# Kernel tuning notes

Measured on AMD Instinct MI355X. Metric: run time of the kernel, lower is better.

Reference implementation:

```python
import jax, jax.numpy as jnp
import numpy as np

B, C, H, W = 128, 256, 32, 32
TD, NHEADS, PH, PW = 192, 4, 4, 4
FF = 384
MAXG = 8
TABLE = (2 * MAXG - 1) ** 2  # 225


def setup_inputs() -> dict:
    key = jax.random.key(0)
    ks = jax.random.split(key, 10)
    rn = lambda k, shape, s=0.02: jax.random.normal(k, shape, jnp.float32) * s
    return {
        "x": jax.random.normal(ks[0], (B, C, H, W), jnp.float32),
        "conv1_w": rn(ks[1], (TD, C)),          # 1x1 conv, no bias
        "conv2_w": rn(ks[2], (C, TD)),          # 1x1 conv, no bias
        "qkv_w": rn(ks[3], (TD, 3 * TD)), "qkv_b": jnp.zeros((3 * TD,), jnp.float32),
        "proj_w": rn(ks[4], (TD, TD)), "proj_b": jnp.zeros((TD,), jnp.float32),
        "ffn_w1": rn(ks[5], (TD, FF)), "ffn_b1": jnp.zeros((FF,), jnp.float32),
        "ffn_w2": rn(ks[6], (FF, TD)), "ffn_b2": jnp.zeros((TD,), jnp.float32),
        "ln1_g": jnp.ones((TD,), jnp.float32), "ln1_b": jnp.zeros((TD,), jnp.float32),
        "ln2_g": jnp.ones((TD,), jnp.float32), "ln2_b": jnp.zeros((TD,), jnp.float32),
        "alpha": rn(ks[7], (1,), 0.1),
        "rpb_table": rn(ks[8], (TABLE, NHEADS)),
    }


def _ln(x, g, b, eps=1e-5):
    m = x.mean(-1, keepdims=True)
    v = ((x - m) ** 2).mean(-1, keepdims=True)
    return (x - m) * jax.lax.rsqrt(v + eps) * g + b


def _rpb_index(Nh, Nw, maxg):
    # static (trace-time) relative position index over the patch grid
    ch, cw = np.meshgrid(np.arange(Nh), np.arange(Nw), indexing="ij")
    coords = np.stack([ch.ravel(), cw.ravel()])                 # (2, N)
    rel = coords[:, :, None] - coords[:, None, :]               # (2, N, N)
    idx = (rel[0] + maxg - 1) * (2 * maxg - 1) + (rel[1] + maxg - 1)
    return jnp.asarray(idx.reshape(-1), jnp.int32)              # (N*N,)


def reference(x, conv1_w, conv2_w, qkv_w, qkv_b, proj_w, proj_b,
              ffn_w1, ffn_b1, ffn_w2, ffn_b2,
              ln1_g, ln1_b, ln2_g, ln2_b, alpha, rpb_table):
    Nh, Nw = H // PH, W // PW
    Np = Nh * Nw
    hd = TD // NHEADS
    scale = 1.0 / np.sqrt(hd).astype(np.float32)

    # local 1x1 conv
    xl = jnp.einsum("bchw,tc->bthw", x, conv1_w)                # (B, TD, H, W)
    # patchify + mean-pool -> one token per patch
    xp = xl.reshape(B, TD, Nh, PH, Nw, PW).transpose(0, 2, 4, 3, 5, 1)
    xp = xp.reshape(B, Np, PH * PW, TD)
    tokens = xp.mean(axis=2)                                    # (B, Np, TD)

    # attention with gathered relative position bias
    t = _ln(tokens, ln1_g, ln1_b)
    qkv = (t @ qkv_w + qkv_b).reshape(B, Np, 3, NHEADS, hd)
    q, k, v = qkv[:, :, 0], qkv[:, :, 1], qkv[:, :, 2]          # (B, Np, H, hd)
    attn = jnp.einsum("bnhd,bmhd->bhnm", q, k) * scale
    bias = rpb_table[_rpb_index(Nh, Nw, MAXG)]                  # (Np*Np, heads)
    bias = bias.reshape(Np, Np, NHEADS).transpose(2, 0, 1)      # (heads, Np, Np)
    attn = jax.nn.softmax(attn + bias[None], axis=-1)
    o = jnp.einsum("bhnm,bmhd->bnhd", attn, v).reshape(B, Np, TD)
    o = o @ proj_w + proj_b

    out = tokens + alpha * o                                    # scaled residual
    h2 = _ln(out, ln2_g, ln2_b)
    out = out + (jax.nn.gelu(h2 @ ffn_w1 + ffn_b1, approximate=False) @ ffn_w2 + ffn_b2)

    # unpatchify: broadcast each token back over its ph*pw pixels
    ot = jnp.broadcast_to(out[:, :, None, :], (B, Np, PH * PW, TD))
    ot = ot.reshape(B, Nh, Nw, PH, PW, TD).transpose(0, 5, 1, 3, 2, 4)
    ot = ot.reshape(B, TD, H, W)
    return x + jnp.einsum("bthw,ct->bchw", ot, conv2_w)
```

## Files before the change

### kernel.cpp

```cpp
#include <hip/hip_runtime.h>
#include <hip/hip_bf16.h>

#define Bsz 128
#define Cch 256
#define Him 32
#define Wim 32
#define TD 192
#define NH 4
#define HD 48
#define FF 384
#define NP 64

typedef float f32x4 __attribute__((ext_vector_type(4)));
typedef __bf16 bf16x8 __attribute__((ext_vector_type(8)));
typedef unsigned int u32;

#define MFMA(a, b, c) __builtin_amdgcn_mfma_f32_16x16x32_bf16(a, b, c, 0, 0, 0)
#define LD8(p) (*reinterpret_cast<const bf16x8*>(p))
#define VM0 asm volatile("s_waitcnt vmcnt(0)" ::: "memory")
#define VM2 asm volatile("s_waitcnt vmcnt(2)" ::: "memory")
#define VMB do { if (wlow) { asm volatile("s_waitcnt vmcnt(4)" ::: "memory"); } \
                 else      { asm volatile("s_waitcnt vmcnt(2)" ::: "memory"); } } while (0)
#define LGKM0 asm volatile("s_waitcnt lgkmcnt(0)" ::: "memory")
#define SBAR __builtin_amdgcn_s_barrier()

__device__ __forceinline__ ushort f2bf(float f) {
    union { __hip_bfloat16 h; ushort u; } cv;
    cv.h = __float2bfloat16(f);
    return cv.u;
}

__device__ __forceinline__ void gload16(const void* g, void* l) {
    __builtin_amdgcn_global_load_lds((const __attribute__((address_space(1))) u32*)g,
                                     (__attribute__((address_space(3))) u32*)l, 16, 0, 0);
}

template <int K2B>
__device__ __forceinline__ void stageW(char* lbuf, const char* g0, int colStrB, int tid) {
    constexpr int CHB = 32 * K2B;
    constexpr int NR = (CHB + 8191) / 8192;
#pragma unroll
    for (int rd = 0; rd < NR; ++rd) {
        int p = rd * 8192 + tid * 16;
        if (p < CHB) {
            int col = p / K2B;
            int kb = (p - col * K2B) ^ ((col & 7) << 4);
            gload16(g0 + (size_t)col * colStrB + kb, lbuf + p);
        }
    }
}

typedef ushort ushort8v __attribute__((ext_vector_type(8)));
__global__ __launch_bounds__(256) void prep_kernel(const float* __restrict__ x,
                                                   const float* __restrict__ c1,
                                                   const float* __restrict__ c2,
                                                   const float* __restrict__ qw,
                                                   const float* __restrict__ pw,
                                                   const float* __restrict__ f1,
                                                   const float* __restrict__ f2,
                                                   ushort* __restrict__ wb,
                                                   ushort* __restrict__ xm) {
    const int bb = blockIdx.x;
    const int tid = threadIdx.x;
    if (bb < 1536) {
        int g = bb * 256 + tid;
        float v;
        if (g < 49152) v = c1[g];
        else if (g < 98304) v = c2[g - 49152];
        else if (g < 208896) { int i = g - 98304;  int n = i / 192, k = i - n * 192; v = qw[k * 576 + n]; }
        else if (g < 245760) { int i = g - 208896; int n = i / 192, k = i - n * 192; v = pw[k * 192 + n]; }
        else if (g < 319488) { int i = g - 245760; int n = i / 192, k = i - n * 192; v = f1[k * 384 + n]; }
        else                 { int i = g - 319488; int n = i / 384, k = i - n * 384; v = f2[k * 192 + n]; }
        wb[g] = f2bf(v);
        return;
    }
    __shared__ float acc[32][65];
    int pb = bb - 1536;
    int b = pb >> 3, cg = pb & 7;
    int c = tid >> 3, wq = tid & 7;
    const float* pl = x + ((size_t)(b * Cch + cg * 32 + c) * 1024) + wq * 4;
#pragma unroll 1
    for (int nh = 0; nh < 8; ++nh) {
        const float* p0 = pl + nh * 128;
        float4 v0 = *reinterpret_cast<const float4*>(p0);
        float4 v1 = *reinterpret_cast<const float4*>(p0 + 32);
        float4 v2 = *reinterpret_cast<const float4*>(p0 + 64);
        float4 v3 = *reinterpret_cast<const float4*>(p0 + 96);
        float s = v0.x + v0.y + v0.z + v0.w + v1.x + v1.y + v1.z + v1.w +
                  v2.x + v2.y + v2.z + v2.w + v3.x + v3.y + v3.z + v3.w;
        acc[c][nh * 8 + wq] = s * 0.0625f;
    }
    __syncthreads();
    int p = tid >> 2, c8 = (tid & 3) * 8;
    ushort8v o;
#pragma unroll
    for (int k = 0; k < 8; ++k) o[k] = f2bf(acc[c8 + k][p]);
    *reinterpret_cast<ushort8v*>(xm + ((size_t)(b * 64 + p)) * 256 + cg * 32 + c8) = o;
}

__global__ __launch_bounds__(512, 1) void token_kernel(
    const ushort* __restrict__ xm, const ushort* __restrict__ wb,
    const float* __restrict__ qkv_b, const float* __restrict__ proj_b,
    const float* __restrict__ ffn_b1, const float* __restrict__ ffn_b2,
    const float* __restrict__ ln1_g, const float* __restrict__ ln1_b,
    const float* __restrict__ ln2_g, const float* __restrict__ ln2_b,
    const float* __restrict__ alphap, const float* __restrict__ rpb,
    ushort* __restrict__ y) {
    __shared__ __align__(16) char LDS[154624];
    ushort* tln = (ushort*)(LDS);
    ushort* qb  = (ushort*)(LDS + 25600);
    ushort* kb  = (ushort*)(LDS + 51200);
    ushort* vT  = (ushort*)(LDS + 76800);
    char*   SBB = LDS + 104448;
    float2* scr2 = (float2*)(LDS + 153600);
    ushort* t2  = tln;
    ushort* obp = qb;
    ushort* h0  = qb;
    ushort* h1  = kb;
    ushort* o2  = vT;
#define SBUF(i) (SBB + (i) * 12288)

    const int b = blockIdx.x;
    const int tid = threadIdx.x, lane = tid & 63, w = tid >> 6;
    const int l15 = lane & 15, slot = lane >> 4, slot16 = slot * 16;
    const int r = w >> 1, cc = w & 1;
    const int rowA = r * 16 + l15;
    const int orow = r * 16 + slot * 4;
    const int xp = (l15 & 7) << 4;
    const int colB = cc * 16 + l15;
    const bool wlow = (w < 4);

    float qbr[18], f1br[12], l1gr[6], l1br[6], l2gr[6], l2br[6], pbr[6], f2br[6];
#pragma unroll
    for (int j = 0; j < 18; ++j) qbr[j] = qkv_b[(j / 6) * 192 + (j % 6) * 32 + colB];
#pragma unroll
    for (int j = 0; j < 12; ++j) f1br[j] = ffn_b1[j * 32 + colB];
#pragma unroll
    for (int c = 0; c < 6; ++c) {
        int col = c * 32 + colB;
        l1gr[c] = ln1_g[col]; l1br[c] = ln1_b[col];
        l2gr[c] = ln2_g[col]; l2br[c] = ln2_b[col];
        pbr[c] = proj_b[col]; f2br[c] = ffn_b2[col];
    }
    const float alpha = alphap[0];

    const char* xrow = (const char*)xm + ((size_t)(b * 64 + rowA)) * 512;
    bf16x8 a1[2][4];
#pragma unroll
    for (int kh = 0; kh < 2; ++kh)
#pragma unroll
        for (int ks = 0; ks < 4; ++ks)
            a1[kh][ks] = LD8(xrow + kh * 256 + ks * 64 + slot16);

    const char* c1g = (const char*)wb;
    const char* qg  = (const char*)(wb + 98304);
    const char* pg  = (const char*)(wb + 208896);
    const char* fg  = (const char*)(wb + 245760);
    const char* f2g = (const char*)(wb + 319488);
    const char* c2g = (const char*)(wb + 49152);

    f32x4 tok[6], pj[6];
#pragma unroll
    for (int c = 0; c < 6; ++c) { tok[c] = f32x4{0,0,0,0}; pj[c] = f32x4{0,0,0,0}; }

    stageW<256>(SBUF(0), c1g, 512, tid);
    stageW<256>(SBUF(1), c1g + 256, 512, tid);
    stageW<256>(SBUF(2), c1g + 16384, 512, tid);
#pragma unroll
    for (int j = 0; j < 12; ++j) {
        if (j < 10) VM2; else VM0;
        SBAR;
        if (j < 9) {
            int jn = j + 3;
            stageW<256>(SBUF(jn & 3), c1g + (size_t)(jn >> 1) * 16384 + (jn & 1) * 256, 512, tid);
        }
        const char* bp = SBUF(j & 3) + colB * 256;
        int c = j >> 1, kh = j & 1;
#pragma unroll
        for (int ks = 0; ks < 4; ++ks)
            tok[c] = MFMA(a1[kh][ks], LD8(bp + ((ks * 64 + slot16) ^ xp)), tok[c]);
    }
    stageW<384>(SBUF(0), qg, 384, tid);
    stageW<384>(SBUF(1), qg + 12288, 384, tid);
    stageW<384>(SBUF(2), qg + 24576, 384, tid);
    {
        float s[4] = {}, s2[4] = {};
#pragma unroll
        for (int c = 0; c < 6; ++c)
#pragma unroll
            for (int j2 = 0; j2 < 4; ++j2) { float v = tok[c][j2]; s[j2] += v; s2[j2] += v * v; }
#pragma unroll
        for (int m = 1; m < 16; m <<= 1)
#pragma unroll
            for (int j2 = 0; j2 < 4; ++j2) { s[j2] += __shfl_xor(s[j2], m); s2[j2] += __shfl_xor(s2[j2], m); }
        if (l15 == 0)
#pragma unroll
            for (int j2 = 0; j2 < 4; ++j2) scr2[(orow + j2) * 2 + cc] = make_float2(s[j2], s2[j2]);
        LGKM0; SBAR;
#pragma unroll
        for (int j2 = 0; j2 < 4; ++j2) {
            int row = orow + j2;
            float2 eA = scr2[row * 2], eB = scr2[row * 2 + 1];
            float mean = (eA.x + eB.x) * (1.f / 192.f);
            float inv = rsqrtf((eA.y + eB.y) * (1.f / 192.f) - mean * mean + 1e-5f);
#pragma unroll
            for (int c = 0; c < 6; ++c)
                tln[row * 200 + c * 32 + colB] = f2bf((tok[c][j2] - mean) * inv * l1gr[c] + l1br[c]);
        }
        LGKM0; SBAR;
    }

    {
        bf16x8 aT[6];
        const char* trow = (const char*)tln + rowA * 400;
#pragma unroll
        for (int ks = 0; ks < 6; ++ks) aT[ks] = LD8(trow + ks * 64 + slot16);
#pragma unroll
        for (int j = 0; j < 18; ++j) {
            if (j < 16) VMB; else VM0;
            SBAR;
            if (j < 15) stageW<384>(SBUF((j + 3) & 3), qg + (size_t)(j + 3) * 12288, 384, tid);
            const char* bp = SBUF(j & 3) + colB * 384;
            f32x4 acc = f32x4{0,0,0,0};
#pragma unroll
            for (int ks = 0; ks < 6; ++ks)
                acc = MFMA(aT[ks], LD8(bp + ((ks * 64 + slot16) ^ xp)), acc);
            int col = (j % 6) * 32 + colB;
            float bias = qbr[j];
            if (j < 6) {
#pragma unroll
                for (int j2 = 0; j2 < 4; ++j2) qb[(orow + j2) * 200 + col] = f2bf(acc[j2] + bias);
            } else if (j < 12) {
#pragma unroll
                for (int j2 = 0; j2 < 4; ++j2) kb[(orow + j2) * 200 + col] = f2bf(acc[j2] + bias);
            } else {
                ushort4 pk;
                pk.x = f2bf(acc[0] + bias); pk.y = f2bf(acc[1] + bias);
                pk.z = f2bf(acc[2] + bias); pk.w = f2bf(acc[3] + bias);
                *reinterpret_cast<ushort4*>(&vT[col * 72 + orow]) = pk;
            }
        }
    }
    LGKM0; SBAR;

    {
        const float scale = 0.14433756729740643f;
        ushort* P2b0 = (ushort*)(LDS + cc * 9216);
        ushort* P2b1 = (ushort*)(LDS + 104448 + cc * 9216);
#pragma unroll
        for (int p = 0; p < 2; ++p) {
            int h = p * 2 + cc;
            ushort* P2 = p ? P2b1 : P2b0;
            float rb[4][4];
#pragma unroll
            for (int j2 = 0; j2 < 4; ++j2) {
                int qrow = orow + j2, qh = qrow >> 3, qw = qrow & 7;
#pragma unroll
                for (int nf = 0; nf < 4; ++nf) {
                    int krow = l15 + nf * 16;
                    rb[j2][nf] = rpb[((qh - (krow >> 3) + 7) * 15 + (qw - (krow & 7) + 7)) * 4 + h];
                }
            }
            uint4 z = make_uint4(0, 0, 0, 0);
            const char* qrp = (const char*)qb + rowA * 400 + h * 96;
            uint4 qa1 = *(const uint4*)(qrp + slot16);
            uint4 qa2 = (slot < 2) ? *(const uint4*)(qrp + 64 + slot16) : z;
            f32x4 S[4] = {};
#pragma unroll
            for (int nf = 0; nf < 4; ++nf) {
                const char* kp = (const char*)kb + (l15 + nf * 16) * 400 + h * 96;
                uint4 k1 = *(const uint4*)(kp + slot16);
                uint4 k2 = (slot < 2) ? *(const uint4*)(kp + 64 + slot16) : z;
                S[nf] = MFMA(*(bf16x8*)&qa1, *(bf16x8*)&k1, S[nf]);
                S[nf] = MFMA(*(bf16x8*)&qa2, *(bf16x8*)&k2, S[nf]);
            }
#pragma unroll
            for (int j2 = 0; j2 < 4; ++j2) {
                float sv[4]; float mx = -1e30f;
#pragma unroll
                for (int nf = 0; nf < 4; ++nf) { sv[nf] = S[nf][j2] * scale + rb[j2][nf]; mx = fmaxf(mx, sv[nf]); }
#pragma unroll
                for (int m = 1; m < 16; m <<= 1) mx = fmaxf(mx, __shfl_xor(mx, m));
                float sum = 0.f;
#pragma unroll
                for (int nf = 0; nf < 4; ++nf) { sv[nf] = expf(sv[nf] - mx); sum += sv[nf]; }
#pragma unroll
                for (int m = 1; m < 16; m <<= 1) sum += __shfl_xor(sum, m);
                float inv = 1.f / sum;
                int qrow = orow + j2;
#pragma unroll
                for (int nf = 0; nf < 4; ++nf) P2[qrow * 72 + l15 + nf * 16] = f2bf(sv[nf] * inv);
            }
        }
        LGKM0; SBAR;
#pragma unroll
        for (int p = 0; p < 2; ++p) {
            int h = p * 2 + cc;
            ushort* P2 = p ? P2b1 : P2b0;
            f32x4 O[3] = {};
            const char* prow = (const char*)P2 + rowA * 144;
#pragma unroll
            for (int ki = 0; ki < 2; ++ki) {
                bf16x8 pa = LD8(prow + ki * 64 + slot16);
#pragma unroll
                for (int nf = 0; nf < 3; ++nf) {
                    bf16x8 vb = LD8((const char*)vT + (h * 48 + l15 + nf * 16) * 144 + ki * 64 + slot16);
                    O[nf] = MFMA(pa, vb, O[nf]);
                }
            }
#pragma unroll
            for (int nf = 0; nf < 3; ++nf)
#pragma unroll
                for (int j2 = 0; j2 < 4; ++j2)
                    obp[(orow + j2) * 200 + h * 48 + l15 + nf * 16] = f2bf(O[nf][j2]);
        }
        LGKM0; SBAR;
    }
    stageW<384>(SBUF(0), pg, 384, tid);
    stageW<384>(SBUF(1), pg + 12288, 384, tid);
    stageW<384>(SBUF(2), pg + 24576, 384, tid);

    {
        bf16x8 aO[6];
        const char* orw = (const char*)obp + rowA * 400;
#pragma unroll
        for (int ks = 0; ks < 6; ++ks) aO[ks] = LD8(orw + ks * 64 + slot16);
#pragma unroll
        for (int j = 0; j < 6; ++j) {
            if (j < 4) VMB; else VM0;
            SBAR;
            if (j < 3) stageW<384>(SBUF((j + 3) & 3), pg + (size_t)(j + 3) * 12288, 384, tid);
            const char* bp = SBUF(j & 3) + colB * 384;
#pragma unroll
            for (int ks = 0; ks < 6; ++ks)
                pj[j] = MFMA(aO[ks], LD8(bp + ((ks * 64 + slot16) ^ xp)), pj[j]);
        }
    }
    SBAR;
    stageW<384>(SBUF(0), fg, 384, tid);
    stageW<384>(SBUF(1), fg + 12288, 384, tid);
    stageW<384>(SBUF(2), fg + 24576, 384, tid);
    {
        float s[4] = {}, s2[4] = {};
#pragma unroll
        for (int c = 0; c < 6; ++c)
#pragma unroll
            for (int j2 = 0; j2 < 4; ++j2) {
                float v = tok[c][j2] + alpha * (pj[c][j2] + pbr[c]);
                pj[c][j2] = v;
                s[j2] += v; s2[j2] += v * v;
            }
#pragma unroll
        for (int m = 1; m < 16; m <<= 1)
#pragma unroll
            for (int j2 = 0; j2 < 4; ++j2) { s[j2] += __shfl_xor(s[j2], m); s2[j2] += __shfl_xor(s2[j2], m); }
        if (l15 == 0)
#pragma unroll
            for (int j2 = 0; j2 < 4; ++j2) scr2[(orow + j2) * 2 + cc] = make_float2(s[j2], s2[j2]);
        LGKM0; SBAR;
#pragma unroll
        for (int j2 = 0; j2 < 4; ++j2) {
            int row = orow + j2;
            float2 eA = scr2[row * 2], eB = scr2[row * 2 + 1];
            float mean = (eA.x + eB.x) * (1.f / 192.f);
            float inv = rsqrtf((eA.y + eB.y) * (1.f / 192.f) - mean * mean + 1e-5f);
#pragma unroll
            for (int c = 0; c < 6; ++c)
                t2[row * 200 + c * 32 + colB] = f2bf((pj[c][j2] - mean) * inv * l2gr[c] + l2br[c]);
        }
        LGKM0; SBAR;
    }

    {
        bf16x8 aT2[6];
        const char* trow = (const char*)t2 + rowA * 400;
#pragma unroll
        for (int ks = 0; ks < 6; ++ks) aT2[ks] = LD8(trow + ks * 64 + slot16);
#pragma unroll
        for (int j = 0; j < 12; ++j) {
            if (j < 10) VMB; else VM0;
            SBAR;
            if (j < 9) stageW<384>(SBUF((j + 3) & 3), fg + (size_t)(j + 3) * 12288, 384, tid);
            const char* bp = SBUF(j & 3) + colB * 384;
            f32x4 acc = f32x4{0,0,0,0};
#pragma unroll
            for (int ks = 0; ks < 6; ++ks)
                acc = MFMA(aT2[ks], LD8(bp + ((ks * 64 + slot16) ^ xp)), acc);
            int col384 = j * 32 + colB;
            ushort* hb = (j < 6) ? h0 : h1;
            int lcol = (j < 6) ? col384 : col384 - 192;
#pragma unroll
            for (int j2 = 0; j2 < 4; ++j2) {
                float v = acc[j2] + f1br[j];
                v = 0.5f * v * (1.f + erff(v * 0.70710678118654752f));
                hb[(orow + j2) * 200 + lcol] = f2bf(v);
            }
        }
    }
    LGKM0; SBAR;
    stageW<384>(SBUF(0), f2g, 768, tid);
    stageW<384>(SBUF(1), f2g + 384, 768, tid);
    stageW<384>(SBUF(2), f2g + 24576, 768, tid);

    f32x4 f2a[6];
#pragma unroll
    for (int c = 0; c < 6; ++c) f2a[c] = f32x4{0,0,0,0};
    {
        bf16x8 ah[2][6];
        const char* h0r = (const char*)h0 + rowA * 400;
        const char* h1r = (const char*)h1 + rowA * 400;
#pragma unroll
        for (int ks = 0; ks < 6; ++ks) {
            ah[0][ks] = LD8(h0r + ks * 64 + slot16);
            ah[1][ks] = LD8(h1r + ks * 64 + slot16);
        }
#pragma unroll
        for (int j = 0; j < 12; ++j) {
            if (j < 10) VMB; else VM0;
            SBAR;
            if (j < 9) {
                int jn = j + 3;
                stageW<384>(SBUF(jn & 3), f2g + (size_t)(jn >> 1) * 24576 + (jn & 1) * 384, 768, tid);
            }
            const char* bp = SBUF(j & 3) + colB * 384;
            int c = j >> 1, kh = j & 1;
#pragma unroll
            for (int ks = 0; ks < 6; ++ks)
                f2a[c] = MFMA(ah[kh][ks], LD8(bp + ((ks * 64 + slot16) ^ xp)), f2a[c]);
        }
    }
    stageW<384>(SBUF(0), c2g, 384, tid);
    stageW<384>(SBUF(1), c2g + 12288, 384, tid);
    stageW<384>(SBUF(2), c2g + 24576, 384, tid);
#pragma unroll
    for (int c = 0; c < 6; ++c) {
        int col = c * 32 + colB;
#pragma unroll
        for (int j2 = 0; j2 < 4; ++j2)
            o2[(orow + j2) * 200 + col] = f2bf(pj[c][j2] + f2a[c][j2] + f2br[c]);
    }
    LGKM0; SBAR;

    {
        bf16x8 aO2[6];
        const char* o2r = (const char*)o2 + rowA * 400;
#pragma unroll
        for (int ks = 0; ks < 6; ++ks) aO2[ks] = LD8(o2r + ks * 64 + slot16);
        ushort* yb = y + (size_t)b * 64 * 256;
#pragma unroll
        for (int j = 0; j < 8; ++j) {
            if (j < 6) VMB; else VM0;
            SBAR;
            if (j < 5) stageW<384>(SBUF((j + 3) & 3), c2g + (size_t)(j + 3) * 12288, 384, tid);
            const char* bp = SBUF(j & 3) + colB * 384;
            f32x4 acc = f32x4{0,0,0,0};
#pragma unroll
            for (int ks = 0; ks < 6; ++ks)
                acc = MFMA(aO2[ks], LD8(bp + ((ks * 64 + slot16) ^ xp)), acc);
            int col = j * 32 + colB;
#pragma unroll
            for (int j2 = 0; j2 < 4; ++j2)
                yb[(size_t)(orow + j2) * 256 + col] = f2bf(acc[j2]);
        }
    }
#undef SBUF
}

__global__ __launch_bounds__(256) void final_kernel(const float* __restrict__ x,
                                                    const ushort* __restrict__ y,
                                                    float* __restrict__ out) {
    size_t g = (size_t)blockIdx.x * 256 + threadIdx.x;
    int w4 = g & 7, hh = (g >> 3) & 31, c = (g >> 8) & 255, b = (int)(g >> 16);
    int p = (hh >> 2) * 8 + w4;
    u32 yu = y[((size_t)b * NP + p) * Cch + c];
    union { u32 u; float f; } cv; cv.u = yu << 16;
    float yv = cv.f;
    f32x4 xv = *(reinterpret_cast<const f32x4*>(x) + g);
    f32x4 ov = {xv.x + yv, xv.y + yv, xv.z + yv, xv.w + yv};
    __builtin_nontemporal_store(ov, reinterpret_cast<f32x4*>(out) + g);
}

extern "C" void kernel_launch(void* const* d_in, const int* in_sizes, int n_in,
                              void* d_out, int out_size, void* d_ws, size_t ws_size,
                              hipStream_t stream) {
    const float* x       = (const float*)d_in[0];
    const float* conv1_w = (const float*)d_in[1];
    const float* conv2_w = (const float*)d_in[2];
    const float* qkv_w   = (const float*)d_in[3];
    const float* qkv_b   = (const float*)d_in[4];
    const float* proj_w  = (const float*)d_in[5];
    const float* proj_b  = (const float*)d_in[6];
    const float* ffn_w1  = (const float*)d_in[7];
    const float* ffn_b1  = (const float*)d_in[8];
    const float* ffn_w2  = (const float*)d_in[9];
    const float* ffn_b2  = (const float*)d_in[10];
    const float* ln1_g   = (const float*)d_in[11];
    const float* ln1_b   = (const float*)d_in[12];
    const float* ln2_g   = (const float*)d_in[13];
    const float* ln2_b   = (const float*)d_in[14];
    const float* alpha   = (const float*)d_in[15];
    const float* rpb     = (const float*)d_in[16];
    float* out = (float*)d_out;

    ushort* ybuf = (ushort*)d_ws;
    ushort* xm   = ybuf + 2097152;
    ushort* wb   = xm + 2097152;

    prep_kernel<<<2560, 256, 0, stream>>>(x, conv1_w, conv2_w, qkv_w, proj_w, ffn_w1, ffn_w2,
                                          wb, xm);
    token_kernel<<<Bsz, 512, 0, stream>>>(xm, wb, qkv_b, proj_b, ffn_b1, ffn_b2,
                                          ln1_g, ln1_b, ln2_g, ln2_b, alpha, rpb, ybuf);
    final_kernel<<<(Bsz * Cch * Him * Wim) / 1024, 256, 0, stream>>>(x, ybuf, out);
}
```

Baseline: 111.2 us.

## Read GEMM weights directly into registers, tile per-wave by 64x16 column strips

The token kernel no longer stages weight tiles into LDS through a triple-buffered global_load_lds pipeline with barriers. Each wave now owns one or two 16-column strips across all 64 rows and loads its B fragments straight from global memory into registers, with the next strip's load software-prefetched. The residual token values move out of registers into a global scratch buffer. This drops LDS staging, most per-step barriers and about 27KB of LDS, at the cost of uncoalesced global weight reads, extra global traffic for the token scratch, and a tail-imbalanced work split (dup12 duplicates the extra strips).

```diff
diff --git a/kernel.cpp b/kernel.cpp
--- a/kernel.cpp
+++ b/kernel.cpp
@@ -14,13 +14,9 @@
 typedef float f32x4 __attribute__((ext_vector_type(4)));
 typedef __bf16 bf16x8 __attribute__((ext_vector_type(8)));
 typedef unsigned int u32;
+typedef ushort ushort8v __attribute__((ext_vector_type(8)));
 
 #define MFMA(a, b, c) __builtin_amdgcn_mfma_f32_16x16x32_bf16(a, b, c, 0, 0, 0)
-#define LD8(p) (*reinterpret_cast<const bf16x8*>(p))
-#define VM0 asm volatile("s_waitcnt vmcnt(0)" ::: "memory")
-#define VM2 asm volatile("s_waitcnt vmcnt(2)" ::: "memory")
-#define VMB do { if (wlow) { asm volatile("s_waitcnt vmcnt(4)" ::: "memory"); } \
-                 else      { asm volatile("s_waitcnt vmcnt(2)" ::: "memory"); } } while (0)
 #define LGKM0 asm volatile("s_waitcnt lgkmcnt(0)" ::: "memory")
 #define SBAR __builtin_amdgcn_s_barrier()
 
@@ -30,27 +26,32 @@
     return cv.u;
 }
 
-__device__ __forceinline__ void gload16(const void* g, void* l) {
-    __builtin_amdgcn_global_load_lds((const __attribute__((address_space(1))) u32*)g,
-                                     (__attribute__((address_space(3))) u32*)l, 16, 0, 0);
-}
-
-template <int K2B>
-__device__ __forceinline__ void stageW(char* lbuf, const char* g0, int colStrB, int tid) {
-    constexpr int CHB = 32 * K2B;
-    constexpr int NR = (CHB + 8191) / 8192;
-#pragma unroll
-    for (int rd = 0; rd < NR; ++rd) {
-        int p = rd * 8192 + tid * 16;
-        if (p < CHB) {
-            int col = p / K2B;
-            int kb = (p - col * K2B) ^ ((col & 7) << 4);
-            gload16(g0 + (size_t)col * colStrB + kb, lbuf + p);
-        }
-    }
-}
-
-typedef ushort ushort8v __attribute__((ext_vector_type(8)));
+__device__ __forceinline__ void loadA6(bf16x8 (&A)[4][6], const ushort* base, int l15, int slot) {
+#pragma unroll
+    for (int rt = 0; rt < 4; ++rt)
+#pragma unroll
+        for (int ks = 0; ks < 6; ++ks)
+            A[rt][ks] = *reinterpret_cast<const bf16x8*>(base + (rt * 16 + l15) * 200 + ks * 32 + slot * 8);
+}
+
+template <int NKS>
+__device__ __forceinline__ void loadB(uint4 (&B)[NKS], const ushort* Wg, int row, int Kel, int kofs, int slot) {
+#pragma unroll
+    for (int ks = 0; ks < NKS; ++ks)
+        B[ks] = *reinterpret_cast<const uint4*>(Wg + (size_t)row * Kel + kofs + ks * 32 + slot * 8);
+}
+
+template <int NKS>
+__device__ __forceinline__ void mfmaStrip(f32x4 (&acc)[4], const bf16x8 (&A)[4][NKS], uint4 (&B)[NKS]) {
+#pragma unroll
+    for (int ks = 0; ks < NKS; ++ks) {
+        bf16x8 bf = *reinterpret_cast<bf16x8*>(&B[ks]);
+#pragma unroll
+        for (int rt = 0; rt < 4; ++rt)
+            acc[rt] = MFMA(A[rt][ks], bf, acc[rt]);
+    }
+}
+
 __global__ __launch_bounds__(256) void prep_kernel(const float* __restrict__ x,
                                                    const float* __restrict__ c1,
                                                    const float* __restrict__ c2,
@@ -105,20 +106,19 @@
     const float* __restrict__ ln1_g, const float* __restrict__ ln1_b,
     const float* __restrict__ ln2_g, const float* __restrict__ ln2_b,
     const float* __restrict__ alphap, const float* __restrict__ rpb,
-    ushort* __restrict__ y) {
-    __shared__ __align__(16) char LDS[154624];
+    float* __restrict__ tokg, ushort* __restrict__ y) {
+    __shared__ __align__(16) char LDS[127488];
     ushort* tln = (ushort*)(LDS);
     ushort* qb  = (ushort*)(LDS + 25600);
     ushort* kb  = (ushort*)(LDS + 51200);
     ushort* vT  = (ushort*)(LDS + 76800);
-    char*   SBB = LDS + 104448;
-    float2* scr2 = (float2*)(LDS + 153600);
+    float2* scrP = (float2*)(LDS + 122880);
+    float2* scrS = (float2*)(LDS + 126976);
     ushort* t2  = tln;
     ushort* obp = qb;
     ushort* h0  = qb;
     ushort* h1  = kb;
     ushort* o2  = vT;
-#define SBUF(i) (SBB + (i) * 12288)
 
     const int b = blockIdx.x;
     const int tid = threadIdx.x, lane = tid & 63, w = tid >> 6;
@@ -126,120 +126,133 @@
     const int r = w >> 1, cc = w & 1;
     const int rowA = r * 16 + l15;
     const int orow = r * 16 + slot * 4;
-    const int xp = (l15 & 7) << 4;
-    const int colB = cc * 16 + l15;
-    const bool wlow = (w < 4);
-
-    float qbr[18], f1br[12], l1gr[6], l1br[6], l2gr[6], l2br[6], pbr[6], f2br[6];
-#pragma unroll
-    for (int j = 0; j < 18; ++j) qbr[j] = qkv_b[(j / 6) * 192 + (j % 6) * 32 + colB];
-#pragma unroll
-    for (int j = 0; j < 12; ++j) f1br[j] = ffn_b1[j * 32 + colB];
-#pragma unroll
-    for (int c = 0; c < 6; ++c) {
-        int col = c * 32 + colB;
-        l1gr[c] = ln1_g[col]; l1br[c] = ln1_b[col];
-        l2gr[c] = ln2_g[col]; l2br[c] = ln2_b[col];
-        pbr[c] = proj_b[col]; f2br[c] = ffn_b2[col];
-    }
+    const int rbase = slot * 4;
     const float alpha = alphap[0];
 
-    const char* xrow = (const char*)xm + ((size_t)(b * 64 + rowA)) * 512;
-    bf16x8 a1[2][4];
-#pragma unroll
-    for (int kh = 0; kh < 2; ++kh)
-#pragma unroll
-        for (int ks = 0; ks < 4; ++ks)
-            a1[kh][ks] = LD8(xrow + kh * 256 + ks * 64 + slot16);
-
-    const char* c1g = (const char*)wb;
-    const char* qg  = (const char*)(wb + 98304);
-    const char* pg  = (const char*)(wb + 208896);
-    const char* fg  = (const char*)(wb + 245760);
-    const char* f2g = (const char*)(wb + 319488);
-    const char* c2g = (const char*)(wb + 49152);
-
-    f32x4 tok[6], pj[6];
-#pragma unroll
-    for (int c = 0; c < 6; ++c) { tok[c] = f32x4{0,0,0,0}; pj[c] = f32x4{0,0,0,0}; }
-
-    stageW<256>(SBUF(0), c1g, 512, tid);
-    stageW<256>(SBUF(1), c1g + 256, 512, tid);
-    stageW<256>(SBUF(2), c1g + 16384, 512, tid);
-#pragma unroll
-    for (int j = 0; j < 12; ++j) {
-        if (j < 10) VM2; else VM0;
-        SBAR;
-        if (j < 9) {
-            int jn = j + 3;
-            stageW<256>(SBUF(jn & 3), c1g + (size_t)(jn >> 1) * 16384 + (jn & 1) * 256, 512, tid);
+    const ushort* c1w   = wb;
+    const ushort* c2w   = wb + 49152;
+    const ushort* qkvT  = wb + 98304;
+    const ushort* projT = wb + 208896;
+    const ushort* f1T   = wb + 245760;
+    const ushort* f2T   = wb + 319488;
+
+    const int sA = w;
+    const int sB = (w + 8 < 12) ? (w + 8) : w;
+    const bool dup12 = (sB == sA);
+    float* tokb = tokg + (size_t)b * 64 * 192;
+
+    f32x4 tok2[2][4] = {};
+#pragma unroll
+    for (int kh = 0; kh < 2; ++kh) {
+        bf16x8 A[4][4];
+#pragma unroll
+        for (int rt = 0; rt < 4; ++rt)
+#pragma unroll
+            for (int ks = 0; ks < 4; ++ks)
+                A[rt][ks] = *reinterpret_cast<const bf16x8*>(
+                    xm + (size_t)(b * 64 + rt * 16 + l15) * 256 + kh * 128 + ks * 32 + slot * 8);
+        uint4 B0[4], B1[4];
+        loadB<4>(B0, c1w, sA * 16 + l15, 256, kh * 128, slot);
+        loadB<4>(B1, c1w, sB * 16 + l15, 256, kh * 128, slot);
+        mfmaStrip<4>(tok2[0], A, B0);
+        mfmaStrip<4>(tok2[1], A, B1);
+    }
+    {
+        float s1v[4][4], s2v[4][4];
+#pragma unroll
+        for (int rt = 0; rt < 4; ++rt)
+#pragma unroll
+            for (int j2 = 0; j2 < 4; ++j2) {
+                float v0 = tok2[0][rt][j2];
+                float v1 = dup12 ? 0.f : tok2[1][rt][j2];
+                s1v[rt][j2] = v0 + v1;
+                s2v[rt][j2] = v0 * v0 + v1 * v1;
+            }
+#pragma unroll
+        for (int m = 1; m < 16; m <<= 1)
+#pragma unroll
+            for (int rt = 0; rt < 4; ++rt)
+#pragma unroll
+                for (int j2 = 0; j2 < 4; ++j2) {
+                    s1v[rt][j2] += __shfl_xor(s1v[rt][j2], m);
+                    s2v[rt][j2] += __shfl_xor(s2v[rt][j2], m);
+                }
+        if (l15 == 0)
+#pragma unroll
+            for (int rt = 0; rt < 4; ++rt)
+#pragma unroll
+                for (int j2 = 0; j2 < 4; ++j2)
+                    scrP[(rt * 16 + rbase + j2) * 8 + w] = make_float2(s1v[rt][j2], s2v[rt][j2]);
+        LGKM0; SBAR;
+        {
+            float sx = 0.f, sy = 0.f;
+#pragma unroll
+            for (int ww = 0; ww < 8; ++ww) { float2 e = scrP[lane * 8 + ww]; sx += e.x; sy += e.y; }
+            float mean = sx * (1.f / 192.f);
+            float inv = rsqrtf(sy * (1.f / 192.f) - mean * mean + 1e-5f);
+            scrS[lane] = make_float2(mean, inv);
         }
-        const char* bp = SBUF(j & 3) + colB * 256;
-        int c = j >> 1, kh = j & 1;
-#pragma unroll
-        for (int ks = 0; ks < 4; ++ks)
-            tok[c] = MFMA(a1[kh][ks], LD8(bp + ((ks * 64 + slot16) ^ xp)), tok[c]);
-    }
-    stageW<384>(SBUF(0), qg, 384, tid);
-    stageW<384>(SBUF(1), qg + 12288, 384, tid);
-    stageW<384>(SBUF(2), qg + 24576, 384, tid);
-    {
-        float s[4] = {}, s2[4] = {};
-#pragma unroll
-        for (int c = 0; c < 6; ++c)
-#pragma unroll
-            for (int j2 = 0; j2 < 4; ++j2) { float v = tok[c][j2]; s[j2] += v; s2[j2] += v * v; }
-#pragma unroll
-        for (int m = 1; m < 16; m <<= 1)
-#pragma unroll
-            for (int j2 = 0; j2 < 4; ++j2) { s[j2] += __shfl_xor(s[j2], m); s2[j2] += __shfl_xor(s2[j2], m); }
-        if (l15 == 0)
-#pragma unroll
-            for (int j2 = 0; j2 < 4; ++j2) scr2[(orow + j2) * 2 + cc] = make_float2(s[j2], s2[j2]);
+        LGKM0;
+        float g0 = ln1_g[sA * 16 + l15], b0 = ln1_b[sA * 16 + l15];
+        float g1 = ln1_g[sB * 16 + l15], b1 = ln1_b[sB * 16 + l15];
+#pragma unroll
+        for (int rt = 0; rt < 4; ++rt)
+#pragma unroll
+            for (int j2 = 0; j2 < 4; ++j2) {
+                int row = rt * 16 + rbase + j2;
+                float2 st = scrS[row];
+                float v0 = tok2[0][rt][j2], v1 = tok2[1][rt][j2];
+                tokb[(size_t)row * 192 + sA * 16 + l15] = v0;
+                tokb[(size_t)row * 192 + sB * 16 + l15] = v1;
+                tln[row * 200 + sA * 16 + l15] = f2bf((v0 - st.x) * st.y * g0 + b0);
+                tln[row * 200 + sB * 16 + l15] = f2bf((v1 - st.x) * st.y * g1 + b1);
+            }
         LGKM0; SBAR;
-#pragma unroll
-        for (int j2 = 0; j2 < 4; ++j2) {
-            int row = orow + j2;
-            float2 eA = scr2[row * 2], eB = scr2[row * 2 + 1];
-            float mean = (eA.x + eB.x) * (1.f / 192.f);
-            float inv = rsqrtf((eA.y + eB.y) * (1.f / 192.f) - mean * mean + 1e-5f);
-#pragma unroll
-            for (int c = 0; c < 6; ++c)
-                tln[row * 200 + c * 32 + colB] = f2bf((tok[c][j2] - mean) * inv * l1gr[c] + l1br[c]);
-        }
-        LGKM0; SBAR;
-    }
-
-    {
-        bf16x8 aT[6];
-        const char* trow = (const char*)tln + rowA * 400;
-#pragma unroll
-        for (int ks = 0; ks < 6; ++ks) aT[ks] = LD8(trow + ks * 64 + slot16);
-#pragma unroll
-        for (int j = 0; j < 18; ++j) {
-            if (j < 16) VMB; else VM0;
-            SBAR;
-            if (j < 15) stageW<384>(SBUF((j + 3) & 3), qg + (size_t)(j + 3) * 12288, 384, tid);
-            const char* bp = SBUF(j & 3) + colB * 384;
-            f32x4 acc = f32x4{0,0,0,0};
-#pragma unroll
-            for (int ks = 0; ks < 6; ++ks)
-                acc = MFMA(aT[ks], LD8(bp + ((ks * 64 + slot16) ^ xp)), acc);
-            int col = (j % 6) * 32 + colB;
-            float bias = qbr[j];
-            if (j < 6) {
-#pragma unroll
-                for (int j2 = 0; j2 < 4; ++j2) qb[(orow + j2) * 200 + col] = f2bf(acc[j2] + bias);
-            } else if (j < 12) {
-#pragma unroll
-                for (int j2 = 0; j2 < 4; ++j2) kb[(orow + j2) * 200 + col] = f2bf(acc[j2] + bias);
+    }
+
+    {
+        bf16x8 A[4][6]; loadA6(A, tln, l15, slot);
+        int sq[5] = { w, w + 8, w + 16, w + 24, (w + 32 < 36) ? w + 32 : w };
+        float bias[5];
+#pragma unroll
+        for (int i = 0; i < 5; ++i) bias[i] = qkv_b[sq[i] * 16 + l15];
+
+        auto epiQKV = [&](int sv, float bv, f32x4 (&acc)[4]) {
+            if (sv < 12) {
+                int col = sv * 16 + l15;
+#pragma unroll
+                for (int rt = 0; rt < 4; ++rt) {
+                    int rb2 = rt * 16 + rbase;
+#pragma unroll
+                    for (int j2 = 0; j2 < 4; ++j2) qb[(rb2 + j2) * 200 + col] = f2bf(acc[rt][j2] + bv);
+                }
+            } else if (sv < 24) {
+                int col = sv * 16 + l15 - 192;
+#pragma unroll
+                for (int rt = 0; rt < 4; ++rt) {
+                    int rb2 = rt * 16 + rbase;
+#pragma unroll
+                    for (int j2 = 0; j2 < 4; ++j2) kb[(rb2 + j2) * 200 + col] = f2bf(acc[rt][j2] + bv);
+                }
             } else {
-                ushort4 pk;
-                pk.x = f2bf(acc[0] + bias); pk.y = f2bf(acc[1] + bias);
-                pk.z = f2bf(acc[2] + bias); pk.w = f2bf(acc[3] + bias);
-                *reinterpret_cast<ushort4*>(&vT[col * 72 + orow]) = pk;
-            }
-        }
+                int c3 = sv * 16 + l15 - 384;
+#pragma unroll
+                for (int rt = 0; rt < 4; ++rt) {
+                    ushort4 pk;
+                    pk.x = f2bf(acc[rt][0] + bv); pk.y = f2bf(acc[rt][1] + bv);
+                    pk.z = f2bf(acc[rt][2] + bv); pk.w = f2bf(acc[rt][3] + bv);
+                    *reinterpret_cast<ushort4*>(&vT[c3 * 72 + rt * 16 + rbase]) = pk;
+                }
+            }
+        };
+        uint4 B0[6], B1[6];
+        loadB<6>(B0, qkvT, sq[0] * 16 + l15, 192, 0, slot);
+        loadB<6>(B1, qkvT, sq[1] * 16 + l15, 192, 0, slot);
+        { f32x4 acc[4] = {}; mfmaStrip<6>(acc, A, B0); loadB<6>(B0, qkvT, sq[2] * 16 + l15, 192, 0, slot); epiQKV(sq[0], bias[0], acc); }
+        { f32x4 acc[4] = {}; mfmaStrip<6>(acc, A, B1); loadB<6>(B1, qkvT, sq[3] * 16 + l15, 192, 0, slot); epiQKV(sq[1], bias[1], acc); }
+        { f32x4 acc[4] = {}; mfmaStrip<6>(acc, A, B0); loadB<6>(B0, qkvT, sq[4] * 16 + l15, 192, 0, slot); epiQKV(sq[2], bias[2], acc); }
+        { f32x4 acc[4] = {}; mfmaStrip<6>(acc, A, B1); epiQKV(sq[3], bias[3], acc); }
+        { f32x4 acc[4] = {}; mfmaStrip<6>(acc, A, B0); epiQKV(sq[4], bias[4], acc); }
     }
     LGKM0; SBAR;
 
@@ -301,10 +314,10 @@
             const char* prow = (const char*)P2 + rowA * 144;
 #pragma unroll
             for (int ki = 0; ki < 2; ++ki) {
-                bf16x8 pa = LD8(prow + ki * 64 + slot16);
+                bf16x8 pa = *reinterpret_cast<const bf16x8*>(prow + ki * 64 + slot16);
 #pragma unroll
                 for (int nf = 0; nf < 3; ++nf) {
-                    bf16x8 vb = LD8((const char*)vT + (h * 48 + l15 + nf * 16) * 144 + ki * 64 + slot16);
+                    bf16x8 vb = *reinterpret_cast<const bf16x8*>((const char*)vT + (h * 48 + l15 + nf * 16) * 144 + ki * 64 + slot16);
                     O[nf] = MFMA(pa, vb, O[nf]);
                 }
             }
@@ -316,154 +329,161 @@
         }
         LGKM0; SBAR;
     }
-    stageW<384>(SBUF(0), pg, 384, tid);
-    stageW<384>(SBUF(1), pg + 12288, 384, tid);
-    stageW<384>(SBUF(2), pg + 24576, 384, tid);
-
-    {
-        bf16x8 aO[6];
-        const char* orw = (const char*)obp + rowA * 400;
-#pragma unroll
-        for (int ks = 0; ks < 6; ++ks) aO[ks] = LD8(orw + ks * 64 + slot16);
-#pragma unroll
-        for (int j = 0; j < 6; ++j) {
-            if (j < 4) VMB; else VM0;
-            SBAR;
-            if (j < 3) stageW<384>(SBUF((j + 3) & 3), pg + (size_t)(j + 3) * 12288, 384, tid);
-            const char* bp = SBUF(j & 3) + colB * 384;
-#pragma unroll
-            for (int ks = 0; ks < 6; ++ks)
-                pj[j] = MFMA(aO[ks], LD8(bp + ((ks * 64 + slot16) ^ xp)), pj[j]);
+
+    float vv[2][4][4];
+    {
+        bf16x8 A[4][6]; loadA6(A, obp, l15, slot);
+        float pb0 = proj_b[sA * 16 + l15], pb1 = proj_b[sB * 16 + l15];
+        uint4 B0[6], B1[6];
+        loadB<6>(B0, projT, sA * 16 + l15, 192, 0, slot);
+        loadB<6>(B1, projT, sB * 16 + l15, 192, 0, slot);
+        f32x4 a0[4] = {}, a1[4] = {};
+        mfmaStrip<6>(a0, A, B0);
+        mfmaStrip<6>(a1, A, B1);
+#pragma unroll
+        for (int rt = 0; rt < 4; ++rt)
+#pragma unroll
+            for (int j2 = 0; j2 < 4; ++j2) {
+                int row = rt * 16 + rbase + j2;
+                size_t gi0 = (size_t)row * 192 + sA * 16 + l15;
+                size_t gi1 = (size_t)row * 192 + sB * 16 + l15;
+                float tv0 = tokb[gi0], tv1 = tokb[gi1];
+                float v0 = tv0 + alpha * (a0[rt][j2] + pb0);
+                float v1 = tv1 + alpha * (a1[rt][j2] + pb1);
+                vv[0][rt][j2] = v0; vv[1][rt][j2] = v1;
+                tokb[gi0] = v0; tokb[gi1] = v1;
+            }
+    }
+    {
+        float s1v[4][4], s2v[4][4];
+#pragma unroll
+        for (int rt = 0; rt < 4; ++rt)
+#pragma unroll
+            for (int j2 = 0; j2 < 4; ++j2) {
+                float v0 = vv[0][rt][j2];
+                float v1 = dup12 ? 0.f : vv[1][rt][j2];
+                s1v[rt][j2] = v0 + v1;
+                s2v[rt][j2] = v0 * v0 + v1 * v1;
+            }
+#pragma unroll
+        for (int m = 1; m < 16; m <<= 1)
+#pragma unroll
+            for (int rt = 0; rt < 4; ++rt)
+#pragma unroll
+                for (int j2 = 0; j2 < 4; ++j2) {
+                    s1v[rt][j2] += __shfl_xor(s1v[rt][j2], m);
+                    s2v[rt][j2] += __shfl_xor(s2v[rt][j2], m);
+                }
+        if (l15 == 0)
+#pragma unroll
+            for (int rt = 0; rt < 4; ++rt)
+#pragma unroll
+                for (int j2 = 0; j2 < 4; ++j2)
+                    scrP[(rt * 16 + rbase + j2) * 8 + w] = make_float2(s1v[rt][j2], s2v[rt][j2]);
+        LGKM0; SBAR;
+        {
+            float sx = 0.f, sy = 0.f;
+#pragma unroll
+            for (int ww = 0; ww < 8; ++ww) { float2 e = scrP[lane * 8 + ww]; sx += e.x; sy += e.y; }
+            float mean = sx * (1.f / 192.f);
+            float inv = rsqrtf(sy * (1.f / 192.f) - mean * mean + 1e-5f);
+            scrS[lane] = make_float2(mean, inv);
         }
-    }
-    SBAR;
-    stageW<384>(SBUF(0), fg, 384, tid);
-    stageW<384>(SBUF(1), fg + 12288, 384, tid);
-    stageW<384>(SBUF(2), fg + 24576, 384, tid);
-    {
-        float s[4] = {}, s2[4] = {};
-#pragma unroll
-        for (int c = 0; c < 6; ++c)
-#pragma unroll
-            for (int j2 = 0; j2 < 4; ++j2) {
-                float v = tok[c][j2] + alpha * (pj[c][j2] + pbr[c]);
-                pj[c][j2] = v;
-                s[j2] += v; s2[j2] += v * v;
-            }
-#pragma unroll
-        for (int m = 1; m < 16; m <<= 1)
-#pragma unroll
-            for (int j2 = 0; j2 < 4; ++j2) { s[j2] += __shfl_xor(s[j2], m); s2[j2] += __shfl_xor(s2[j2], m); }
-        if (l15 == 0)
-#pragma unroll
-            for (int j2 = 0; j2 < 4; ++j2) scr2[(orow + j2) * 2 + cc] = make_float2(s[j2], s2[j2]);
+        LGKM0;
+        float g0 = ln2_g[sA * 16 + l15], b0 = ln2_b[sA * 16 + l15];
+        float g1 = ln2_g[sB * 16 + l15], b1 = ln2_b[sB * 16 + l15];
+#pragma unroll
+        for (int rt = 0; rt < 4; ++rt)
+#pragma unroll
+            for (int j2 = 0; j2 < 4; ++j2) {
+                int row = rt * 16 + rbase + j2;
+                float2 st = scrS[row];
+                t2[row * 200 + sA * 16 + l15] = f2bf((vv[0][rt][j2] - st.x) * st.y * g0 + b0);
+                t2[row * 200 + sB * 16 + l15] = f2bf((vv[1][rt][j2] - st.x) * st.y * g1 + b1);
+            }
         LGKM0; SBAR;
-#pragma unroll
-        for (int j2 = 0; j2 < 4; ++j2) {
-            int row = orow + j2;
-            float2 eA = scr2[row * 2], eB = scr2[row * 2 + 1];
-            float mean = (eA.x + eB.x) * (1.f / 192.f);
-            float inv = rsqrtf((eA.y + eB.y) * (1.f / 192.f) - mean * mean + 1e-5f);
-#pragma unroll
-            for (int c = 0; c < 6; ++c)
-                t2[row * 200 + c * 32 + colB] = f2bf((pj[c][j2] - mean) * inv * l2gr[c] + l2br[c]);
+    }
+
+    {
+        bf16x8 A[4][6]; loadA6(A, t2, l15, slot);
+        int sf[3] = { w, w + 8, w + 16 };
+        float fb[3];
+#pragma unroll
+        for (int i = 0; i < 3; ++i) fb[i] = ffn_b1[sf[i] * 16 + l15];
+        auto epiF1 = [&](int sv, float bv, f32x4 (&acc)[4]) {
+            ushort* hb = (sv < 12) ? h0 : h1;
+            int col = ((sv < 12) ? sv * 16 : (sv - 12) * 16) + l15;
+#pragma unroll
+            for (int rt = 0; rt < 4; ++rt) {
+                int rb2 = rt * 16 + rbase;
+#pragma unroll
+                for (int j2 = 0; j2 < 4; ++j2) {
+                    float v = acc[rt][j2] + bv;
+                    v = 0.5f * v * (1.f + erff(v * 0.70710678118654752f));
+                    hb[(rb2 + j2) * 200 + col] = f2bf(v);
+                }
+            }
+        };
+        uint4 B0[6], B1[6];
+        loadB<6>(B0, f1T, sf[0] * 16 + l15, 192, 0, slot);
+        loadB<6>(B1, f1T, sf[1] * 16 + l15, 192, 0, slot);
+        { f32x4 acc[4] = {}; mfmaStrip<6>(acc, A, B0); loadB<6>(B0, f1T, sf[2] * 16 + l15, 192, 0, slot); epiF1(sf[0], fb[0], acc); }
+        { f32x4 acc[4] = {}; mfmaStrip<6>(acc, A, B1); epiF1(sf[1], fb[1], acc); }
+        { f32x4 acc[4] = {}; mfmaStrip<6>(acc, A, B0); epiF1(sf[2], fb[2], acc); }
+    }
+    LGKM0; SBAR;
+
+    f32x4 f2a0[4] = {}, f2a1[4] = {};
+    {
+        {
+            bf16x8 A[4][6]; loadA6(A, h0, l15, slot);
+            uint4 B0[6], B1[6];
+            loadB<6>(B0, f2T, sA * 16 + l15, 384, 0, slot);
+            loadB<6>(B1, f2T, sB * 16 + l15, 384, 0, slot);
+            mfmaStrip<6>(f2a0, A, B0);
+            mfmaStrip<6>(f2a1, A, B1);
         }
-        LGKM0; SBAR;
-    }
-
-    {
-        bf16x8 aT2[6];
-        const char* trow = (const char*)t2 + rowA * 400;
-#pragma unroll
-        for (int ks = 0; ks < 6; ++ks) aT2[ks] = LD8(trow + ks * 64 + slot16);
-#pragma unroll
-        for (int j = 0; j < 12; ++j) {
-            if (j < 10) VMB; else VM0;
-            SBAR;
-            if (j < 9) stageW<384>(SBUF((j + 3) & 3), fg + (size_t)(j + 3) * 12288, 384, tid);
-            const char* bp = SBUF(j & 3) + colB * 384;
-            f32x4 acc = f32x4{0,0,0,0};
-#pragma unroll
-            for (int ks = 0; ks < 6; ++ks)
-                acc = MFMA(aT2[ks], LD8(bp + ((ks * 64 + slot16) ^ xp)), acc);
-            int col384 = j * 32 + colB;
-            ushort* hb = (j < 6) ? h0 : h1;
-            int lcol = (j < 6) ? col384 : col384 - 192;
-#pragma unroll
-            for (int j2 = 0; j2 < 4; ++j2) {
-                float v = acc[j2] + f1br[j];
-                v = 0.5f * v * (1.f + erff(v * 0.70710678118654752f));
-                hb[(orow + j2) * 200 + lcol] = f2bf(v);
-            }
+        {
+            bf16x8 A[4][6]; loadA6(A, h1, l15, slot);
+            uint4 B0[6], B1[6];
+            loadB<6>(B0, f2T, sA * 16 + l15, 384, 192, slot);
+            loadB<6>(B1, f2T, sB * 16 + l15, 384, 192, slot);
+            mfmaStrip<6>(f2a0, A, B0);
+            mfmaStrip<6>(f2a1, A, B1);
         }
+        float fb0 = ffn_b2[sA * 16 + l15], fb1 = ffn_b2[sB * 16 + l15];
+#pragma unroll
+        for (int rt = 0; rt < 4; ++rt)
+#pragma unroll
+            for (int j2 = 0; j2 < 4; ++j2) {
+                int row = rt * 16 + rbase + j2;
+                float o0 = tokb[(size_t)row * 192 + sA * 16 + l15] + f2a0[rt][j2] + fb0;
+                float o1 = tokb[(size_t)row * 192 + sB * 16 + l15] + f2a1[rt][j2] + fb1;
+                o2[row * 200 + sA * 16 + l15] = f2bf(o0);
+                o2[row * 200 + sB * 16 + l15] = f2bf(o1);
+            }
     }
     LGKM0; SBAR;
-    stageW<384>(SBUF(0), f2g, 768, tid);
-    stageW<384>(SBUF(1), f2g + 384, 768, tid);
-    stageW<384>(SBUF(2), f2g + 24576, 768, tid);
-
-    f32x4 f2a[6];
-#pragma unroll
-    for (int c = 0; c < 6; ++c) f2a[c] = f32x4{0,0,0,0};
-    {
-        bf16x8 ah[2][6];
-        const char* h0r = (const char*)h0 + rowA * 400;
-        const char* h1r = (const char*)h1 + rowA * 400;
-#pragma unroll
-        for (int ks = 0; ks < 6; ++ks) {
-            ah[0][ks] = LD8(h0r + ks * 64 + slot16);
-            ah[1][ks] = LD8(h1r + ks * 64 + slot16);
-        }
-#pragma unroll
-        for (int j = 0; j < 12; ++j) {
-            if (j < 10) VMB; else VM0;
-            SBAR;
-            if (j < 9) {
-                int jn = j + 3;
-                stageW<384>(SBUF(jn & 3), f2g + (size_t)(jn >> 1) * 24576 + (jn & 1) * 384, 768, tid);
-            }
-            const char* bp = SBUF(j & 3) + colB * 384;
-            int c = j >> 1, kh = j & 1;
-#pragma unroll
-            for (int ks = 0; ks < 6; ++ks)
-                f2a[c] = MFMA(ah[kh][ks], LD8(bp + ((ks * 64 + slot16) ^ xp)), f2a[c]);
-        }
-    }
-    stageW<384>(SBUF(0), c2g, 384, tid);
-    stageW<384>(SBUF(1), c2g + 12288, 384, tid);
-    stageW<384>(SBUF(2), c2g + 24576, 384, tid);
-#pragma unroll
-    for (int c = 0; c < 6; ++c) {
-        int col = c * 32 + colB;
-#pragma unroll
-        for (int j2 = 0; j2 < 4; ++j2)
-            o2[(orow + j2) * 200 + col] = f2bf(pj[c][j2] + f2a[c][j2] + f2br[c]);
-    }
-    LGKM0; SBAR;
-
-    {
-        bf16x8 aO2[6];
-        const char* o2r = (const char*)o2 + rowA * 400;
-#pragma unroll
-        for (int ks = 0; ks < 6; ++ks) aO2[ks] = LD8(o2r + ks * 64 + slot16);
+
+    {
+        bf16x8 A[4][6]; loadA6(A, o2, l15, slot);
+        int t0 = w, t1 = w + 8;
+        uint4 B0[6], B1[6];
+        loadB<6>(B0, c2w, t0 * 16 + l15, 192, 0, slot);
+        loadB<6>(B1, c2w, t1 * 16 + l15, 192, 0, slot);
+        f32x4 a0[4] = {}, a1[4] = {};
+        mfmaStrip<6>(a0, A, B0);
+        mfmaStrip<6>(a1, A, B1);
         ushort* yb = y + (size_t)b * 64 * 256;
 #pragma unroll
-        for (int j = 0; j < 8; ++j) {
-            if (j < 6) VMB; else VM0;
-            SBAR;
-            if (j < 5) stageW<384>(SBUF((j + 3) & 3), c2g + (size_t)(j + 3) * 12288, 384, tid);
-            const char* bp = SBUF(j & 3) + colB * 384;
-            f32x4 acc = f32x4{0,0,0,0};
-#pragma unroll
-            for (int ks = 0; ks < 6; ++ks)
-                acc = MFMA(aO2[ks], LD8(bp + ((ks * 64 + slot16) ^ xp)), acc);
-            int col = j * 32 + colB;
-#pragma unroll
-            for (int j2 = 0; j2 < 4; ++j2)
-                yb[(size_t)(orow + j2) * 256 + col] = f2bf(acc[j2]);
-        }
-    }
-#undef SBUF
+        for (int rt = 0; rt < 4; ++rt)
+#pragma unroll
+            for (int j2 = 0; j2 < 4; ++j2) {
+                int row = rt * 16 + rbase + j2;
+                yb[(size_t)row * 256 + t0 * 16 + l15] = f2bf(a0[rt][j2]);
+                yb[(size_t)row * 256 + t1 * 16 + l15] = f2bf(a1[rt][j2]);
+            }
+    }
 }
 
 __global__ __launch_bounds__(256) void final_kernel(const float* __restrict__ x,
@@ -505,10 +525,11 @@
     ushort* ybuf = (ushort*)d_ws;
     ushort* xm   = ybuf + 2097152;
     ushort* wb   = xm + 2097152;
+    float*  tokg = (float*)(wb + 393216);
 
     prep_kernel<<<2560, 256, 0, stream>>>(x, conv1_w, conv2_w, qkv_w, proj_w, ffn_w1, ffn_w2,
                                           wb, xm);
     token_kernel<<<Bsz, 512, 0, stream>>>(xm, wb, qkv_b, proj_b, ffn_b1, ffn_b2,
-                                          ln1_g, ln1_b, ln2_g, ln2_b, alpha, rpb, ybuf);
+                                          ln1_g, ln1_b, ln2_g, ln2_b, alpha, rpb, tokg, ybuf);
     final_kernel<<<(Bsz * Cch * Him * Wim) / 1024, 256, 0, stream>>>(x, ybuf, out);
 }
```

Result: slower. 159.1 us (+43.1%).
